# Kernel optimization log

Hardware: AMD Instinct MI355X
Metric: run time of the kernel (lower is better)

The kernel has to match this reference:

```python
import jax, jax.numpy as jnp
import numpy as np

B, L, D = 8, 2048, 64   # batch, length, input_dim
K, NU = 40, 32          # num scales, reservoir units
LEAKY = 0.0
REG = 1.0


def setup_inputs() -> dict:
    key = jax.random.key(0)
    k1, k2 = jax.random.split(key)
    x = jax.random.normal(k1, (B, L, D), dtype=jnp.float32)
    radii = jax.random.uniform(k2, (K,), dtype=jnp.float32, minval=0.1, maxval=0.99)
    rng = np.random.default_rng(0)
    W_in = jnp.asarray(rng.standard_normal((D, NU)).astype(np.float32))
    # uni_res=True: one sparse reservoir, spectral-radius normalized, repeated K times
    connectivity = min(1.0, 10.0 / NU)
    w = rng.standard_normal((NU, NU)) * (rng.random((NU, NU)) < connectivity)
    w = w / np.max(np.abs(np.linalg.eigvals(w)))
    W_res = jnp.asarray(np.repeat(w[None].astype(np.float32), K, axis=0))
    return {"x": x, "radii": radii, "W_in": W_in, "W_res": W_res}


def reference(x, radii, W_in, W_res):
    Bb, Ll, Dd = x.shape
    k, nu = W_res.shape[0], W_res.shape[1]
    T = Ll - 1
    xt = x @ W_in                                # [B,L,nu]
    Wr = W_res * radii[:, None, None]            # [k,nu,nu]
    ar = jnp.arange(k)

    # Multi-scale recurrence: scale r reads its own state delayed by r+1 steps.
    # Rolling buffer buf[:, r, j] holds column (t-1-j) of scale r's history, so
    # h_pre for scale r is the diagonal buf[:, r, r] (== h_history[:, r, t-r-1];
    # zero for t-r-1 < 0, matching the torch code's untouched zero init).
    def step(buf, x_t):                          # buf [B,k,k,nu], x_t [B,nu]
        h_pre = buf[:, ar, ar, :]                # [B,k,nu] diagonal gather
        h_t = x_t[:, None, :] + jnp.einsum('brn,rnm->brm', h_pre, Wr)
        new = LEAKY * h_pre + (1.0 - LEAKY) * jnp.tanh(h_t)
        buf = jnp.concatenate([new[:, :, None, :], buf[:, :, :-1, :]], axis=2)
        return buf, new

    buf0 = jnp.zeros((Bb, k, k, nu), x.dtype)
    _, hist = jax.lax.scan(step, buf0, jnp.swapaxes(xt[:, :T], 0, 1))
    h_hist = jnp.transpose(hist, (1, 2, 0, 3))   # [B,k,T,nu]

    # Scale i has L-1-i valid timesteps; mask instead of ragged slicing.
    t_idx = jnp.arange(T)
    mask = (t_idx[None, :] < (Ll - 1 - ar)[:, None]).astype(x.dtype)  # [k,T]
    Hm = h_hist * mask[None, :, :, None]          # [B,k,T,nu]
    idx = jnp.minimum(t_idx[None, :] + ar[:, None] + 1, Ll - 1)       # [k,T]
    Xm = x[:, idx, :] * mask[None, :, :, None]    # [B,k,T,D] (x shifted by i+1)

    eye = REG * jnp.eye(nu, dtype=x.dtype)
    HtH = jnp.einsum('bktn,bktm->bknm', Hm, Hm) + eye   # [B,k,nu,nu]
    HtX = jnp.einsum('bktn,bktd->bknd', Hm, Xm)         # [B,k,nu,D]
    W_out = jnp.linalg.solve(HtH, HtX)                  # [B,k,nu,D]

    err = jnp.einsum('bktn,bknd->bktd', Hm, W_out) - Xm
    f_norms = jnp.sum(err, axis=(0, 2, 3))              # [k]
    features = W_out.reshape(Bb, k, nu * Dd)            # [B,k,nu*D]
    return features, f_norms
```

## Files before the change

### kernel.cpp

```cpp
#include <hip/hip_runtime.h>

#define B_ 8
#define L_ 2048
#define D_ 64
#define K_ 40
#define NU_ 32
#define T_ 2047
#define NSPLIT 8

#define XT_OFF   0
#define XT_SZ    (B_*L_*NU_)
#define HH_OFF   (XT_OFF + XT_SZ)
#define HH_SZ    (B_*K_*T_*NU_)
#define HTHP_OFF (HH_OFF + HH_SZ)
#define HTHP_SZ  (NSPLIT*B_*K_*NU_*NU_)
#define HTXP_OFF (HTHP_OFF + HTHP_SZ)
#define HTXP_SZ  (NSPLIT*B_*K_*NU_*D_)
#define SH_OFF   (HTXP_OFF + HTXP_SZ)
#define SH_SZ    (B_*K_*NU_)
#define SX_OFF   (SH_OFF + SH_SZ)
#define SX_SZ    (B_*K_)

#if __has_builtin(__builtin_amdgcn_exp2f)
#define EXP2F(x) __builtin_amdgcn_exp2f(x)
#else
#define EXP2F(x) __expf((x)*0.6931471805599453f)
#endif
#if __has_builtin(__builtin_amdgcn_rcpf)
#define RCPF(x) __builtin_amdgcn_rcpf(x)
#else
#define RCPF(x) (1.0f/(x))
#endif

__global__ __launch_bounds__(256) void k1_xt(const float* __restrict__ x,
                                             const float* __restrict__ Win,
                                             float* __restrict__ xt)
{
    __shared__ float Ws[D_*NU_];
    for (int i = threadIdx.x; i < D_*NU_; i += 256) Ws[i] = Win[i];
    __syncthreads();
    int gid = blockIdx.x*256 + threadIdx.x;
    int m   = gid & 31;
    int row = gid >> 5;
    const float4* xr = (const float4*)(x + (size_t)row * 64);
    float s = 0.f;
#pragma unroll
    for (int q = 0; q < 16; ++q) {
        float4 v = xr[q];
        s = fmaf(v.x, Ws[(q*4+0)*32+m], s);
        s = fmaf(v.y, Ws[(q*4+1)*32+m], s);
        s = fmaf(v.z, Ws[(q*4+2)*32+m], s);
        s = fmaf(v.w, Ws[(q*4+3)*32+m], s);
    }
    xt[gid] = s;
}

#define RLV(N) __int_as_float(__builtin_amdgcn_readlane(hb, N))

#define STEP(XV, SD) { \
    float a0 = XV, a1 = 0.f, a2 = 0.f, a3 = 0.f; \
    a0 = fmaf(w0,  RLV(0),  a0); a1 = fmaf(w1,  RLV(1),  a1); \
    a2 = fmaf(w2,  RLV(2),  a2); a3 = fmaf(w3,  RLV(3),  a3); \
    a0 = fmaf(w4,  RLV(4),  a0); a1 = fmaf(w5,  RLV(5),  a1); \
    a2 = fmaf(w6,  RLV(6),  a2); a3 = fmaf(w7,  RLV(7),  a3); \
    a0 = fmaf(w8,  RLV(8),  a0); a1 = fmaf(w9,  RLV(9),  a1); \
    a2 = fmaf(w10, RLV(10), a2); a3 = fmaf(w11, RLV(11), a3); \
    a0 = fmaf(w12, RLV(12), a0); a1 = fmaf(w13, RLV(13), a1); \
    a2 = fmaf(w14, RLV(14), a2); a3 = fmaf(w15, RLV(15), a3); \
    a0 = fmaf(w16, RLV(16), a0); a1 = fmaf(w17, RLV(17), a1); \
    a2 = fmaf(w18, RLV(18), a2); a3 = fmaf(w19, RLV(19), a3); \
    a0 = fmaf(w20, RLV(20), a0); a1 = fmaf(w21, RLV(21), a1); \
    a2 = fmaf(w22, RLV(22), a2); a3 = fmaf(w23, RLV(23), a3); \
    a0 = fmaf(w24, RLV(24), a0); a1 = fmaf(w25, RLV(25), a1); \
    a2 = fmaf(w26, RLV(26), a2); a3 = fmaf(w27, RLV(27), a3); \
    a0 = fmaf(w28, RLV(28), a0); a1 = fmaf(w29, RLV(29), a1); \
    a2 = fmaf(w30, RLV(30), a2); a3 = fmaf(w31, RLV(31), a3); \
    float sdot = (a0 + a1) + (a2 + a3); \
    float ex = EXP2F(sdot * 2.8853900817779268f); \
    SD = fmaf(-2.f, RCPF(ex + 1.f), 1.f); \
    hb = __float_as_int(SD); }

#define CHUNK(XC, XN, ST) { \
    XN##0 = xnp[0];               XN##1 = xnp[(size_t)1*adv]; \
    XN##2 = xnp[(size_t)2*adv];   XN##3 = xnp[(size_t)3*adv]; \
    XN##4 = xnp[(size_t)4*adv];   XN##5 = xnp[(size_t)5*adv]; \
    XN##6 = xnp[(size_t)6*adv];   XN##7 = xnp[(size_t)7*adv]; \
    xnp += 8*(size_t)adv; \
    STEP(XC##0, ST##0) STEP(XC##1, ST##1) STEP(XC##2, ST##2) STEP(XC##3, ST##3) \
    STEP(XC##4, ST##4) STEP(XC##5, ST##5) STEP(XC##6, ST##6) STEP(XC##7, ST##7) \
    if (l < 32) { \
        if (srem > 0) hq[0]             = ST##0; \
        if (srem > 1) hq[(size_t)1*adv] = ST##1; \
        if (srem > 2) hq[(size_t)2*adv] = ST##2; \
        if (srem > 3) hq[(size_t)3*adv] = ST##3; \
        if (srem > 4) hq[(size_t)4*adv] = ST##4; \
        if (srem > 5) hq[(size_t)5*adv] = ST##5; \
        if (srem > 6) hq[(size_t)6*adv] = ST##6; \
        if (srem > 7) hq[(size_t)7*adv] = ST##7; \
    } \
    hq += 8*(size_t)adv; srem -= 8; }

__global__ __launch_bounds__(64, 2) void k2_rec(const float* __restrict__ ws_xt,
                                                const float* __restrict__ Wres,
                                                const float* __restrict__ radii,
                                                float* __restrict__ hh)
{
    const int l = threadIdx.x;
    const int m = l & 31;
    int e = blockIdx.x % 820;
    int b = blockIdx.x / 820;
    int r = 0, base = 0;
    while (e >= base + r + 1) { base += r + 1; ++r; }
    const int cc     = e - base;
    const int stride = r + 1;
    const float rad  = radii[r];
    const float* Wp = Wres + r*1024 + m;
    float w0  = Wp[0*32]*rad,  w1  = Wp[1*32]*rad,  w2  = Wp[2*32]*rad,  w3  = Wp[3*32]*rad;
    float w4  = Wp[4*32]*rad,  w5  = Wp[5*32]*rad,  w6  = Wp[6*32]*rad,  w7  = Wp[7*32]*rad;
    float w8  = Wp[8*32]*rad,  w9  = Wp[9*32]*rad,  w10 = Wp[10*32]*rad, w11 = Wp[11*32]*rad;
    float w12 = Wp[12*32]*rad, w13 = Wp[13*32]*rad, w14 = Wp[14*32]*rad, w15 = Wp[15*32]*rad;
    float w16 = Wp[16*32]*rad, w17 = Wp[17*32]*rad, w18 = Wp[18*32]*rad, w19 = Wp[19*32]*rad;
    float w20 = Wp[20*32]*rad, w21 = Wp[21*32]*rad, w22 = Wp[22*32]*rad, w23 = Wp[23*32]*rad;
    float w24 = Wp[24*32]*rad, w25 = Wp[25*32]*rad, w26 = Wp[26*32]*rad, w27 = Wp[27*32]*rad;
    float w28 = Wp[28*32]*rad, w29 = Wp[29*32]*rad, w30 = Wp[30*32]*rad, w31 = Wp[31*32]*rad;

    const float* xt = ws_xt + (size_t)b * L_ * NU_;
    float* hrow = hh + ((size_t)(b*K_ + r)) * T_ * NU_;

    const int nsteps = (T_ - 1 - cc) / stride + 1;
    const int adv = stride * NU_;
    const float* xnp = xt + (size_t)cc * NU_ + m;
    float* hq = hrow + (size_t)cc * NU_ + m;

    float xa0 = xnp[0],             xa1 = xnp[(size_t)1*adv],
          xa2 = xnp[(size_t)2*adv], xa3 = xnp[(size_t)3*adv],
          xa4 = xnp[(size_t)4*adv], xa5 = xnp[(size_t)5*adv],
          xa6 = xnp[(size_t)6*adv], xa7 = xnp[(size_t)7*adv];
    xnp += 8*(size_t)adv;
    float xb0=0,xb1=0,xb2=0,xb3=0,xb4=0,xb5=0,xb6=0,xb7=0;
    float sa0,sa1,sa2,sa3,sa4,sa5,sa6,sa7;
    float sb0,sb1,sb2,sb3,sb4,sb5,sb6,sb7;

    int hb = 0;
    int srem = nsteps;
    const int nchunks = (nsteps + 7) >> 3;
    int c = 0;
    for (; c + 2 <= nchunks; c += 2) {
        CHUNK(xa, xb, sa)
        CHUNK(xb, xa, sb)
    }
    if (c < nchunks) CHUNK(xa, xb, sa)
}

__global__ __launch_bounds__(64) void k3_gemm(const float* __restrict__ hh,
                                              const float* __restrict__ x,
                                              float* __restrict__ htHp,
                                              float* __restrict__ htXp,
                                              float* __restrict__ sH,
                                              float* __restrict__ sX)
{
    const int s  = blockIdx.x;
    const int k  = blockIdx.y;
    const int b  = blockIdx.z;
    const int l  = threadIdx.x;
    const int bk = b*K_ + k;
    const int Tk = T_ - k;
    __shared__ __align__(16) float P[32][96];
    const int tidn = l / 12;
    const int tidc = l % 12;

    float acc[8][8];
#pragma unroll
    for (int i = 0; i < 8; ++i)
#pragma unroll
        for (int j = 0; j < 8; ++j) acc[i][j] = 0.f;
    float bsum[8];
#pragma unroll
    for (int j = 0; j < 8; ++j) bsum[j] = 0.f;

    const float* hrow = hh + (size_t)bk * T_ * NU_;
    const float* xrow = x + (size_t)b * L_ * D_ + (size_t)(k+1) * D_;

    for (int ch = s*8; ch < s*8 + 8; ++ch) {
        const int t0 = ch*32;
#pragma unroll
        for (int rd = 0; rd < 12; ++rd) {
            int slot = rd*64 + l;
            int row  = slot / 24;
            int q    = slot % 24;
            int tt   = t0 + row;
            float4 v = make_float4(0.f, 0.f, 0.f, 0.f);
            if (tt < Tk) {
                if (q < 8) v = *(const float4*)(hrow + (size_t)tt*32 + q*4);
                else       v = *(const float4*)(xrow + (size_t)tt*64 + (q-8)*4);
            }
            *(float4*)&P[row][q*4] = v;
        }
        __syncthreads();
        if (l < 48) {
#pragma unroll 4
            for (int tt = 0; tt < 32; ++tt) {
                const float* pr = &P[tt][0];
                float4 A0 = *(const float4*)(pr + tidn*8);
                float4 A1 = *(const float4*)(pr + tidn*8 + 4);
                float4 B0 = *(const float4*)(pr + tidc*8);
                float4 B1 = *(const float4*)(pr + tidc*8 + 4);
                float av[8] = {A0.x,A0.y,A0.z,A0.w,A1.x,A1.y,A1.z,A1.w};
                float bv[8] = {B0.x,B0.y,B0.z,B0.w,B1.x,B1.y,B1.z,B1.w};
#pragma unroll
                for (int i = 0; i < 8; ++i)
#pragma unroll
                    for (int j = 0; j < 8; ++j)
                        acc[i][j] = fmaf(av[i], bv[j], acc[i][j]);
#pragma unroll
                for (int j = 0; j < 8; ++j) bsum[j] += bv[j];
            }
        }
        __syncthreads();
    }
    if (l < 48) {
        const int base_h = (s*(B_*K_) + bk)*NU_*NU_;
        const int base_x = (s*(B_*K_) + bk)*NU_*D_;
#pragma unroll
        for (int i = 0; i < 8; ++i) {
            int n = tidn*8 + i;
#pragma unroll
            for (int j = 0; j < 8; ++j) {
                int c = tidc*8 + j;
                if (c < 32) htHp[base_h + n*32 + c]      = acc[i][j];
                else        htXp[base_x + n*64 + (c-32)] = acc[i][j];
            }
        }
        if (tidn == 0) {
            if (tidc < 4) {
#pragma unroll
                for (int j = 0; j < 8; ++j)
                    atomicAdd(&sH[bk*32 + tidc*8 + j], bsum[j]);
            } else {
                float t = 0.f;
#pragma unroll
                for (int j = 0; j < 8; ++j) t += bsum[j];
                atomicAdd(&sX[bk], t);
            }
        }
    }
}

__global__ __launch_bounds__(64) void k4_solve(const float* __restrict__ htHp,
                                               const float* __restrict__ htXp,
                                               const float* __restrict__ sH,
                                               const float* __restrict__ sX,
                                               float* __restrict__ dout)
{
    const int k  = blockIdx.x;
    const int b  = blockIdx.y;
    const int bk = b*K_ + k;
    const int l  = threadIdx.x;
    __shared__ float As[32][33];
#pragma unroll
    for (int i = 0; i < 16; ++i) {
        int idx = i*64 + l;
        int row = idx >> 5, col = idx & 31;
        float v = (row == col) ? 1.0f : 0.0f;
        for (int s2 = 0; s2 < NSPLIT; ++s2)
            v += htHp[(size_t)(s2*(B_*K_) + bk)*1024 + idx];
        As[row][col] = v;
    }
    __syncthreads();
    for (int j = 0; j < 32; ++j) {
        float d   = sqrtf(As[j][j]);
        float inv = 1.0f / d;
        if (l == j) As[j][j] = d;
        if (l < 32 && l > j) As[l][j] *= inv;
        __syncthreads();
        if (l < 32 && l > j) {
            float lij = As[l][j];
            for (int c = j+1; c <= l; ++c)
                As[l][c] -= lij * As[c][j];
        }
        __syncthreads();
    }
    float y[32];
#pragma unroll
    for (int i = 0; i < 32; ++i) {
        float v = 0.f;
        for (int s2 = 0; s2 < NSPLIT; ++s2)
            v += htXp[(size_t)(s2*(B_*K_) + bk)*2048 + i*64 + l];
        y[i] = v;
    }
#pragma unroll
    for (int i = 0; i < 32; ++i) {
        float v = y[i];
#pragma unroll
        for (int j = 0; j < i; ++j) v = fmaf(-As[i][j], y[j], v);
        y[i] = v / As[i][i];
    }
#pragma unroll
    for (int i = 31; i >= 0; --i) {
        float v = y[i];
#pragma unroll
        for (int j = i+1; j < 32; ++j) v = fmaf(-As[j][i], y[j], v);
        y[i] = v / As[i][i];
    }
    float* fout = dout + (size_t)bk * NU_ * D_;
#pragma unroll
    for (int n = 0; n < 32; ++n) fout[n*64 + l] = y[n];
    const float* sh = sH + bk*32;
    float part = 0.f;
#pragma unroll
    for (int n = 0; n < 32; ++n) part = fmaf(sh[n], y[n], part);
#pragma unroll
    for (int off = 32; off > 0; off >>= 1) part += __shfl_xor(part, off);
    if (l == 0) atomicAdd(dout + (size_t)(B_*K_*NU_*D_) + k, part - sX[bk]);
}

extern "C" void kernel_launch(void* const* d_in, const int* in_sizes, int n_in,
                              void* d_out, int out_size, void* d_ws, size_t ws_size,
                              hipStream_t stream)
{
    const float* x     = (const float*)d_in[0];
    const float* radii = (const float*)d_in[1];
    const float* Win   = (const float*)d_in[2];
    const float* Wres  = (const float*)d_in[3];
    float* ws   = (float*)d_ws;
    float* xt   = ws + XT_OFF;
    float* hh   = ws + HH_OFF;
    float* htHp = ws + HTHP_OFF;
    float* htXp = ws + HTXP_OFF;
    float* sH   = ws + SH_OFF;
    float* sX   = ws + SX_OFF;
    float* out  = (float*)d_out;

    hipMemsetAsync(sH, 0, (size_t)(SH_SZ + SX_SZ)*sizeof(float), stream);
    hipMemsetAsync(out + (size_t)B_*K_*NU_*D_, 0, K_*sizeof(float), stream);

    k1_xt <<<(B_*L_*NU_)/256, 256, 0, stream>>>(x, Win, xt);
    k2_rec<<<B_*820, 64, 0, stream>>>(xt, Wres, radii, hh);
    k3_gemm<<<dim3(NSPLIT, K_, B_), 64, 0, stream>>>(hh, x, htHp, htXp, sH, sX);
    k4_solve<<<dim3(K_, B_), 64, 0, stream>>>(htHp, htXp, sH, sX, out);
}
```

Before: 909.2 us.

## Pack two batches per wavefront in recurrence via ds_bpermute and prioritize long chains

The recurrence kernel previously used only the lower 32 lanes of each 64-lane wave, broadcasting state with readlane. Now each half-wave handles a different batch element, broadcasting state within each half with ds_bpermute, which halves the number of blocks. Blocks for small-stride scales, which have the longest serial chains, get higher wave priority via s_setprio. The trade-off is that ds_bpermute goes through the LDS crossbar and has higher latency than readlane on a serial dependency chain, which could lengthen each step.

```diff
diff --git a/kernel.cpp b/kernel.cpp
--- a/kernel.cpp
+++ b/kernel.cpp
@@ -55,26 +55,26 @@
     xt[gid] = s;
 }
 
-#define RLV(N) __int_as_float(__builtin_amdgcn_readlane(hb, N))
+#define BPV(N) __int_as_float(__builtin_amdgcn_ds_bpermute(pbase + ((N)<<2), hb))
 
 #define STEP(XV, SD) { \
     float a0 = XV, a1 = 0.f, a2 = 0.f, a3 = 0.f; \
-    a0 = fmaf(w0,  RLV(0),  a0); a1 = fmaf(w1,  RLV(1),  a1); \
-    a2 = fmaf(w2,  RLV(2),  a2); a3 = fmaf(w3,  RLV(3),  a3); \
-    a0 = fmaf(w4,  RLV(4),  a0); a1 = fmaf(w5,  RLV(5),  a1); \
-    a2 = fmaf(w6,  RLV(6),  a2); a3 = fmaf(w7,  RLV(7),  a3); \
-    a0 = fmaf(w8,  RLV(8),  a0); a1 = fmaf(w9,  RLV(9),  a1); \
-    a2 = fmaf(w10, RLV(10), a2); a3 = fmaf(w11, RLV(11), a3); \
-    a0 = fmaf(w12, RLV(12), a0); a1 = fmaf(w13, RLV(13), a1); \
-    a2 = fmaf(w14, RLV(14), a2); a3 = fmaf(w15, RLV(15), a3); \
-    a0 = fmaf(w16, RLV(16), a0); a1 = fmaf(w17, RLV(17), a1); \
-    a2 = fmaf(w18, RLV(18), a2); a3 = fmaf(w19, RLV(19), a3); \
-    a0 = fmaf(w20, RLV(20), a0); a1 = fmaf(w21, RLV(21), a1); \
-    a2 = fmaf(w22, RLV(22), a2); a3 = fmaf(w23, RLV(23), a3); \
-    a0 = fmaf(w24, RLV(24), a0); a1 = fmaf(w25, RLV(25), a1); \
-    a2 = fmaf(w26, RLV(26), a2); a3 = fmaf(w27, RLV(27), a3); \
-    a0 = fmaf(w28, RLV(28), a0); a1 = fmaf(w29, RLV(29), a1); \
-    a2 = fmaf(w30, RLV(30), a2); a3 = fmaf(w31, RLV(31), a3); \
+    a0 = fmaf(w0,  BPV(0),  a0); a1 = fmaf(w1,  BPV(1),  a1); \
+    a2 = fmaf(w2,  BPV(2),  a2); a3 = fmaf(w3,  BPV(3),  a3); \
+    a0 = fmaf(w4,  BPV(4),  a0); a1 = fmaf(w5,  BPV(5),  a1); \
+    a2 = fmaf(w6,  BPV(6),  a2); a3 = fmaf(w7,  BPV(7),  a3); \
+    a0 = fmaf(w8,  BPV(8),  a0); a1 = fmaf(w9,  BPV(9),  a1); \
+    a2 = fmaf(w10, BPV(10), a2); a3 = fmaf(w11, BPV(11), a3); \
+    a0 = fmaf(w12, BPV(12), a0); a1 = fmaf(w13, BPV(13), a1); \
+    a2 = fmaf(w14, BPV(14), a2); a3 = fmaf(w15, BPV(15), a3); \
+    a0 = fmaf(w16, BPV(16), a0); a1 = fmaf(w17, BPV(17), a1); \
+    a2 = fmaf(w18, BPV(18), a2); a3 = fmaf(w19, BPV(19), a3); \
+    a0 = fmaf(w20, BPV(20), a0); a1 = fmaf(w21, BPV(21), a1); \
+    a2 = fmaf(w22, BPV(22), a2); a3 = fmaf(w23, BPV(23), a3); \
+    a0 = fmaf(w24, BPV(24), a0); a1 = fmaf(w25, BPV(25), a1); \
+    a2 = fmaf(w26, BPV(26), a2); a3 = fmaf(w27, BPV(27), a3); \
+    a0 = fmaf(w28, BPV(28), a0); a1 = fmaf(w29, BPV(29), a1); \
+    a2 = fmaf(w30, BPV(30), a2); a3 = fmaf(w31, BPV(31), a3); \
     float sdot = (a0 + a1) + (a2 + a3); \
     float ex = EXP2F(sdot * 2.8853900817779268f); \
     SD = fmaf(-2.f, RCPF(ex + 1.f), 1.f); \
@@ -88,7 +88,12 @@
     xnp += 8*(size_t)adv; \
     STEP(XC##0, ST##0) STEP(XC##1, ST##1) STEP(XC##2, ST##2) STEP(XC##3, ST##3) \
     STEP(XC##4, ST##4) STEP(XC##5, ST##5) STEP(XC##6, ST##6) STEP(XC##7, ST##7) \
-    if (l < 32) { \
+    if (srem >= 8) { \
+        hq[0]             = ST##0; hq[(size_t)1*adv] = ST##1; \
+        hq[(size_t)2*adv] = ST##2; hq[(size_t)3*adv] = ST##3; \
+        hq[(size_t)4*adv] = ST##4; hq[(size_t)5*adv] = ST##5; \
+        hq[(size_t)6*adv] = ST##6; hq[(size_t)7*adv] = ST##7; \
+    } else { \
         if (srem > 0) hq[0]             = ST##0; \
         if (srem > 1) hq[(size_t)1*adv] = ST##1; \
         if (srem > 2) hq[(size_t)2*adv] = ST##2; \
@@ -96,7 +101,6 @@
         if (srem > 4) hq[(size_t)4*adv] = ST##4; \
         if (srem > 5) hq[(size_t)5*adv] = ST##5; \
         if (srem > 6) hq[(size_t)6*adv] = ST##6; \
-        if (srem > 7) hq[(size_t)7*adv] = ST##7; \
     } \
     hq += 8*(size_t)adv; srem -= 8; }
 
@@ -105,15 +109,23 @@
                                                 const float* __restrict__ radii,
                                                 float* __restrict__ hh)
 {
-    const int l = threadIdx.x;
-    const int m = l & 31;
+    const int l    = threadIdx.x;
+    const int m    = l & 31;
+    const int half = l >> 5;
+    const int pbase = half << 7;
     int e = blockIdx.x % 820;
-    int b = blockIdx.x / 820;
+    int q = blockIdx.x / 820;
+    const int b = 2*q + half;
     int r = 0, base = 0;
     while (e >= base + r + 1) { base += r + 1; ++r; }
     const int cc     = e - base;
     const int stride = r + 1;
     const float rad  = radii[r];
+
+    if (r == 0)      __builtin_amdgcn_s_setprio(3);
+    else if (r <= 2) __builtin_amdgcn_s_setprio(2);
+    else if (r <= 6) __builtin_amdgcn_s_setprio(1);
+
     const float* Wp = Wres + r*1024 + m;
     float w0  = Wp[0*32]*rad,  w1  = Wp[1*32]*rad,  w2  = Wp[2*32]*rad,  w3  = Wp[3*32]*rad;
     float w4  = Wp[4*32]*rad,  w5  = Wp[5*32]*rad,  w6  = Wp[6*32]*rad,  w7  = Wp[7*32]*rad;
@@ -124,13 +136,10 @@
     float w24 = Wp[24*32]*rad, w25 = Wp[25*32]*rad, w26 = Wp[26*32]*rad, w27 = Wp[27*32]*rad;
     float w28 = Wp[28*32]*rad, w29 = Wp[29*32]*rad, w30 = Wp[30*32]*rad, w31 = Wp[31*32]*rad;
 
-    const float* xt = ws_xt + (size_t)b * L_ * NU_;
-    float* hrow = hh + ((size_t)(b*K_ + r)) * T_ * NU_;
-
     const int nsteps = (T_ - 1 - cc) / stride + 1;
     const int adv = stride * NU_;
-    const float* xnp = xt + (size_t)cc * NU_ + m;
-    float* hq = hrow + (size_t)cc * NU_ + m;
+    const float* xnp = ws_xt + (size_t)b * L_ * NU_ + (size_t)cc * NU_ + m;
+    float* hq = hh + ((size_t)(b*K_ + r) * T_ + cc) * NU_ + m;
 
     float xa0 = xnp[0],             xa1 = xnp[(size_t)1*adv],
           xa2 = xnp[(size_t)2*adv], xa3 = xnp[(size_t)3*adv],
@@ -335,7 +344,7 @@
     hipMemsetAsync(out + (size_t)B_*K_*NU_*D_, 0, K_*sizeof(float), stream);
 
     k1_xt <<<(B_*L_*NU_)/256, 256, 0, stream>>>(x, Win, xt);
-    k2_rec<<<B_*820, 64, 0, stream>>>(xt, Wres, radii, hh);
+    k2_rec<<<4*820, 64, 0, stream>>>(xt, Wres, radii, hh);
     k3_gemm<<<dim3(NSPLIT, K_, B_), 64, 0, stream>>>(hh, x, htHp, htXp, sH, sX);
     k4_solve<<<dim3(K_, B_), 64, 0, stream>>>(htHp, htXp, sH, sX, out);
 }
```

New measurement: 935.6 us. 2.9% more time.
